# Kernel tuning notes

Measured on AMD Instinct MI355X. Metric: run time of the kernel, lower is better.

Reference implementation:

```python
import jax, jax.numpy as jnp
import numpy as np

B, T, C = 4, 2048, 1024
H = 16
D = C // H  # head_dim = 64
SCALE = D ** -0.5


def setup_inputs() -> dict:
    key = jax.random.key(0)
    k1, k2, k3 = jax.random.split(key, 3)
    x = jax.random.normal(k1, (B, T, C), dtype=jnp.float32)
    w_qkv = jax.random.normal(k2, (C, 3 * C), dtype=jnp.float32) * (C ** -0.5)
    w_proj = jax.random.normal(k3, (C, C), dtype=jnp.float32) * (C ** -0.5)
    return {"x": x, "w_qkv": w_qkv, "w_proj": w_proj}


def reference(x, w_qkv, w_proj):
    Bx, Tx, Cx = x.shape
    qkv = x @ w_qkv                        # [B, T, 3C]
    q, k, v = jnp.split(qkv, 3, axis=-1)   # each [B, T, C]
    # [B, T, H, D] -> [B, H, T, D]
    q = q.reshape(Bx, Tx, H, D).transpose(0, 2, 1, 3)
    k = k.reshape(Bx, Tx, H, D).transpose(0, 2, 1, 3)
    v = v.reshape(Bx, Tx, H, D).transpose(0, 2, 1, 3)
    att = jnp.einsum('bhqd,bhkd->bhqk', q, k) * SCALE  # [B, H, T, T]
    causal = jnp.tril(jnp.ones((Tx, Tx), dtype=bool))
    att = jnp.where(causal[None, None], att, -jnp.inf)
    att = jax.nn.softmax(att, axis=-1)
    # dropout p=0.0 (eval-mode reference): identity
    y = jnp.einsum('bhqk,bhkd->bhqd', att, v)          # [B, H, T, D]
    y = y.transpose(0, 2, 1, 3).reshape(Bx, Tx, Cx)    # [B, T, C]
    return y @ w_proj
```

## Files before the change

kernel.cpp:

```cpp
#include <hip/hip_runtime.h>
#include <hip/hip_bf16.h>

#define Bdim 4
#define Tdim 2048
#define Cdim 1024
#define Hdim 16
#define Ddim 64
#define SCALE_Q 0.125f

using f32x4  = __attribute__((ext_vector_type(4))) float;
using short8 = __attribute__((ext_vector_type(8))) short;

union U8 { uint4 v; unsigned short s[8]; };

__device__ __forceinline__ float bf2f(unsigned short u) {
  union { unsigned int i; float f; } x; x.i = ((unsigned int)u) << 16; return x.f;
}
__device__ __forceinline__ unsigned short f2bf(float f) {
  union { float f; unsigned int i; } x; x.f = f;
  unsigned int lsb = (x.i >> 16) & 1u;
  unsigned int r = x.i + 0x7fffu + lsb;
  return (unsigned short)(r >> 16);
}

__device__ __forceinline__ void glds16(const unsigned short* g, unsigned short* l) {
  __builtin_amdgcn_global_load_lds(
      (const __attribute__((address_space(1))) void*)g,
      (__attribute__((address_space(3))) void*)l,
      16, 0, 0);
}

__global__ void detect_kernel(const unsigned int* __restrict__ x, int* __restrict__ flag) {
  if (threadIdx.x == 0) {
    int cnt = 0;
    for (int i = 0; i < 64; i++) {
      unsigned int e = (x[i] >> 7) & 0xFFu;
      if (e >= 100u && e <= 140u) cnt++;
    }
    *flag = (cnt >= 40) ? 1 : 0;
  }
}

__global__ __launch_bounds__(256) void cvt_kernel(
    const void* __restrict__ src, unsigned short* __restrict__ dst,
    const int* __restrict__ flag, size_t n8)
{
  const size_t i = (size_t)blockIdx.x * 256 + threadIdx.x;
  if (i >= n8) return;
  if (*flag == 1) {
    *(uint4*)(dst + i * 8) = *(const uint4*)((const unsigned short*)src + i * 8);
  } else {
    const float* s = (const float*)src + i * 8;
    float4 a = *(const float4*)(s);
    float4 b = *(const float4*)(s + 4);
    U8 o;
    o.s[0]=f2bf(a.x); o.s[1]=f2bf(a.y); o.s[2]=f2bf(a.z); o.s[3]=f2bf(a.w);
    o.s[4]=f2bf(b.x); o.s[5]=f2bf(b.y); o.s[6]=f2bf(b.z); o.s[7]=f2bf(b.w);
    *(uint4*)(dst + i * 8) = o.v;
  }
}

__global__ __launch_bounds__(256) void cvtT_kernel(
    const void* __restrict__ W, unsigned short* __restrict__ WT,
    const int* __restrict__ flag, int K, int N)
{
  __shared__ __align__(16) unsigned short Ts[64][72];
  const int fmt = *flag;
  const int tid = threadIdx.x;
  const int n0 = blockIdx.x * 64, k0 = blockIdx.y * 64;
  const int r = tid >> 2, c0 = (tid & 3) * 16;

  if (fmt == 0) {
    const float* Wf = (const float*)W + (size_t)(k0 + r) * N + n0 + c0;
    #pragma unroll
    for (int j4 = 0; j4 < 4; j4++) {
      float4 v = *(const float4*)(Wf + j4 * 4);
      Ts[r][c0 + j4*4 + 0] = f2bf(v.x);
      Ts[r][c0 + j4*4 + 1] = f2bf(v.y);
      Ts[r][c0 + j4*4 + 2] = f2bf(v.z);
      Ts[r][c0 + j4*4 + 3] = f2bf(v.w);
    }
  } else {
    const unsigned short* Wh = (const unsigned short*)W + (size_t)(k0 + r) * N + n0 + c0;
    uint4 v0 = *(const uint4*)(Wh);
    uint4 v1 = *(const uint4*)(Wh + 8);
    *(uint4*)&Ts[r][c0] = v0;
    *(uint4*)&Ts[r][c0 + 8] = v1;
  }
  __syncthreads();

  U8 o0, o1;
  #pragma unroll
  for (int j = 0; j < 8; j++) { o0.s[j] = Ts[c0 + j][r]; o1.s[j] = Ts[c0 + 8 + j][r]; }
  unsigned short* dst = WT + (size_t)(n0 + r) * K + k0 + c0;
  *(uint4*)(dst)     = o0.v;
  *(uint4*)(dst + 8) = o1.v;
}

__global__ __launch_bounds__(256) void vtrans_kernel(
    const unsigned short* __restrict__ Vb, unsigned short* __restrict__ VbT)
{
  __shared__ __align__(16) unsigned short Ts[64][72];
  const int tid = threadIdx.x;
  const int head = blockIdx.x >> 5;
  const int tt   = blockIdx.x & 31;
  const int r = tid >> 2, c0 = (tid & 3) * 16;

  const unsigned short* src = Vb + (size_t)head * Tdim * Ddim + (size_t)(tt * 64 + r) * Ddim + c0;
  uint4 a = *(const uint4*)(src);
  uint4 b = *(const uint4*)(src + 8);
  *(uint4*)&Ts[r][c0]     = a;
  *(uint4*)&Ts[r][c0 + 8] = b;
  __syncthreads();

  U8 o0, o1;
  #pragma unroll
  for (int j = 0; j < 8; j++) { o0.s[j] = Ts[c0 + j][r]; o1.s[j] = Ts[c0 + 8 + j][r]; }
  unsigned short* dst = VbT + (size_t)head * Tdim * Ddim + (size_t)r * Tdim + tt * 64 + c0;
  *(uint4*)(dst)     = o0.v;
  *(uint4*)(dst + 8) = o1.v;
}

__global__ __launch_bounds__(256) void gemm128a_kernel(
    const unsigned short* __restrict__ A16,
    const unsigned short* __restrict__ BT16,
    void* __restrict__ Cout,
    unsigned short* __restrict__ Qb,
    unsigned short* __restrict__ Kb,
    unsigned short* __restrict__ Vb,
    const int* __restrict__ flag,
    int M, int N, int K, int mode)
{
  __shared__ __align__(16) unsigned short As[128 * 32];
  __shared__ __align__(16) unsigned short Bs[128 * 32];

  const int fmt = *flag;
  const int tid  = threadIdx.x;
  const int wave = tid >> 6;
  const int lane = tid & 63;
  const int col  = lane & 15;
  const int quad = lane >> 4;
  const int m0 = blockIdx.x * 128;
  const int n0 = blockIdx.y * 128;
  const int wm = (wave >> 1) * 64;
  const int wn = (wave & 1) * 64;

  const int lr = lane >> 2;
  const int lc = (lane & 3) * 8;

  f32x4 acc[4][4];
  #pragma unroll
  for (int i = 0; i < 4; i++)
    #pragma unroll
    for (int j = 0; j < 4; j++) acc[i][j] = (f32x4){0.f, 0.f, 0.f, 0.f};

  for (int k0 = 0; k0 < K; k0 += 32) {
    #pragma unroll
    for (int j = 0; j < 2; j++) {
      const int row = wave * 32 + j * 16;
      glds16(A16  + (size_t)(m0 + row + lr) * K + k0 + lc, &As[row * 32]);
      glds16(BT16 + (size_t)(n0 + row + lr) * K + k0 + lc, &Bs[row * 32]);
    }
    __syncthreads();

    short8 afr[4], bfr[4];
    #pragma unroll
    for (int mi = 0; mi < 4; mi++)
      afr[mi] = *(const short8*)&As[(wm + mi * 16 + col) * 32 + quad * 8];
    #pragma unroll
    for (int ni = 0; ni < 4; ni++)
      bfr[ni] = *(const short8*)&Bs[(wn + ni * 16 + col) * 32 + quad * 8];
    #pragma unroll
    for (int mi = 0; mi < 4; mi++)
      #pragma unroll
      for (int ni = 0; ni < 4; ni++)
        acc[mi][ni] = __builtin_amdgcn_mfma_f32_16x16x32_bf16(afr[mi], bfr[ni], acc[mi][ni], 0, 0, 0);
    __syncthreads();
  }

  #pragma unroll
  for (int mi = 0; mi < 4; mi++) {
    #pragma unroll
    for (int ni = 0; ni < 4; ni++) {
      #pragma unroll
      for (int i = 0; i < 4; i++) {
        const int m = m0 + wm + mi * 16 + quad * 4 + i;
        const int n = n0 + wn + ni * 16 + col;
        const float v = acc[mi][ni][i];
        if (mode == 0) {
          if (fmt == 0) ((float*)Cout)[(size_t)m * N + n] = v;
          else ((unsigned short*)Cout)[(size_t)m * N + n] = f2bf(v);
        } else {
          const int which = n >> 10;
          const int rem = n & 1023;
          const int h = rem >> 6;
          const int d = rem & 63;
          const int b = m >> 11;
          const int t = m & 2047;
          const size_t idx = ((size_t)(b * Hdim + h) * Tdim + t) * Ddim + d;
          if      (which == 0) Qb[idx] = f2bf(v * SCALE_Q);
          else if (which == 1) Kb[idx] = f2bf(v);
          else                 Vb[idx] = f2bf(v);
        }
      }
    }
  }
}

#define XBM 128
#define XBN 128
#define XBK 32
#define XLDK 40

__global__ __launch_bounds__(256) void gemm128_kernel(
    const unsigned short* __restrict__ A16,
    const void* __restrict__ Bsrc,
    void* __restrict__ Cout,
    unsigned short* __restrict__ Qb,
    unsigned short* __restrict__ Kb,
    unsigned short* __restrict__ Vb,
    const int* __restrict__ flag,
    int M, int N, int K, int mode, int bFmt)
{
  __shared__ __align__(16) unsigned short As[XBM * XLDK];
  __shared__ __align__(16) unsigned short Bs[XBN * XLDK];

  const int fmt = *flag;
  const int tid  = threadIdx.x;
  const int wave = tid >> 6;
  const int lane = tid & 63;
  const int col  = lane & 15;
  const int quad = lane >> 4;
  const int m0 = blockIdx.x * XBM;
  const int n0 = blockIdx.y * XBN;
  const int wm = (wave >> 1) * 64;
  const int wn = (wave & 1) * 64;

  const int ar = tid >> 1;
  const int ah = (tid & 1) * 16;

  f32x4 acc[4][4];
  #pragma unroll
  for (int i = 0; i < 4; i++)
    #pragma unroll
    for (int j = 0; j < 4; j++) acc[i][j] = (f32x4){0.f, 0.f, 0.f, 0.f};

  for (int k0 = 0; k0 < K; k0 += XBK) {
    {
      const unsigned short* Ap = A16 + (size_t)(m0 + ar) * K + k0 + ah;
      uint4 a0 = *(const uint4*)(Ap);
      uint4 a1 = *(const uint4*)(Ap + 8);
      *(uint4*)&As[ar * XLDK + ah]     = a0;
      *(uint4*)&As[ar * XLDK + ah + 8] = a1;
    }
    if (bFmt == 1) {
      const unsigned short* Bp = (const unsigned short*)Bsrc + (size_t)(n0 + ar) * K + k0 + ah;
      uint4 b0 = *(const uint4*)(Bp);
      uint4 b1 = *(const uint4*)(Bp + 8);
      *(uint4*)&Bs[ar * XLDK + ah]     = b0;
      *(uint4*)&Bs[ar * XLDK + ah + 8] = b1;
    } else {
      const int bn = tid & 127;
      const int bg = (tid >> 7) * 16;
      U8 p0, p1;
      if (fmt == 0) {
        const float* Bf = (const float*)Bsrc;
        #pragma unroll
        for (int j = 0; j < 8; j++) {
          p0.s[j] = f2bf(Bf[(size_t)(k0 + bg + j) * N + n0 + bn]);
          p1.s[j] = f2bf(Bf[(size_t)(k0 + bg + 8 + j) * N + n0 + bn]);
        }
      } else {
        const unsigned short* Bh = (const unsigned short*)Bsrc;
        #pragma unroll
        for (int j = 0; j < 8; j++) {
          p0.s[j] = Bh[(size_t)(k0 + bg + j) * N + n0 + bn];
          p1.s[j] = Bh[(size_t)(k0 + bg + 8 + j) * N + n0 + bn];
        }
      }
      *(uint4*)&Bs[bn * XLDK + bg]     = p0.v;
      *(uint4*)&Bs[bn * XLDK + bg + 8] = p1.v;
    }
    __syncthreads();

    short8 afr[4], bfr[4];
    #pragma unroll
    for (int mi = 0; mi < 4; mi++)
      afr[mi] = *(const short8*)&As[(wm + mi * 16 + col) * XLDK + quad * 8];
    #pragma unroll
    for (int ni = 0; ni < 4; ni++)
      bfr[ni] = *(const short8*)&Bs[(wn + ni * 16 + col) * XLDK + quad * 8];
    #pragma unroll
    for (int mi = 0; mi < 4; mi++)
      #pragma unroll
      for (int ni = 0; ni < 4; ni++)
        acc[mi][ni] = __builtin_amdgcn_mfma_f32_16x16x32_bf16(afr[mi], bfr[ni], acc[mi][ni], 0, 0, 0);
    __syncthreads();
  }

  #pragma unroll
  for (int mi = 0; mi < 4; mi++) {
    #pragma unroll
    for (int ni = 0; ni < 4; ni++) {
      #pragma unroll
      for (int i = 0; i < 4; i++) {
        const int m = m0 + wm + mi * 16 + quad * 4 + i;
        const int n = n0 + wn + ni * 16 + col;
        const float v = acc[mi][ni][i];
        if (mode == 0) {
          if (fmt == 0) ((float*)Cout)[(size_t)m * N + n] = v;
          else ((unsigned short*)Cout)[(size_t)m * N + n] = f2bf(v);
        } else {
          const int which = n >> 10;
          const int rem = n & 1023;
          const int h = rem >> 6;
          const int d = rem & 63;
          const int b = m >> 11;
          const int t = m & 2047;
          const size_t idx = ((size_t)(b * Hdim + h) * Tdim + t) * Ddim + d;
          if      (which == 0) Qb[idx] = f2bf(v * SCALE_Q);
          else if (which == 1) Kb[idx] = f2bf(v);
          else                 Vb[idx] = f2bf(v);
        }
      }
    }
  }
}

#define BM 64
#define BN 64
#define BK 32
#define LDK 40

__global__ __launch_bounds__(256) void gemm64_kernel(
    const void* __restrict__ A,
    const void* __restrict__ Bw,
    void* __restrict__ Cout,
    unsigned short* __restrict__ Qb,
    unsigned short* __restrict__ Kb,
    unsigned short* __restrict__ Vb,
    const int* __restrict__ flag,
    int M, int N, int K, int mode, int aFmt, int outFmt, int aOff, int mOff)
{
  __shared__ __align__(16) unsigned short As[BM * LDK];
  __shared__ __align__(16) unsigned short Bs[BN * LDK];

  const int fmt = *flag;
  const int af  = (aFmt  == 2) ? fmt : aFmt;
  const int of  = (outFmt == 2) ? fmt : outFmt;

  const int tid  = threadIdx.x;
  const int wave = tid >> 6;
  const int lane = tid & 63;
  const int m0 = blockIdx.x * BM;
  const int n0 = blockIdx.y * BN;

  const int ar = tid >> 2;
  const int ak = (tid & 3) * 8;
  const int bk = tid >> 3;
  const int bn = (tid & 7) * 8;

  const int lr = lane & 15;
  const int lq = lane >> 4;

  f32x4 acc[4] = {{0,0,0,0},{0,0,0,0},{0,0,0,0},{0,0,0,0}};

  for (int k0 = 0; k0 < K; k0 += BK) {
    U8 a8;
    if (af == 1) {
      a8.v = *(const uint4*)((const unsigned short*)A + (size_t)(aOff + m0 + ar) * K + (k0 + ak));
    } else {
      const float* Af = (const float*)A + (size_t)(aOff + m0 + ar) * K + (k0 + ak);
      float4 x0 = *(const float4*)(Af);
      float4 x1 = *(const float4*)(Af + 4);
      a8.s[0] = f2bf(x0.x); a8.s[1] = f2bf(x0.y); a8.s[2] = f2bf(x0.z); a8.s[3] = f2bf(x0.w);
      a8.s[4] = f2bf(x1.x); a8.s[5] = f2bf(x1.y); a8.s[6] = f2bf(x1.z); a8.s[7] = f2bf(x1.w);
    }
    *(uint4*)(&As[ar * LDK + ak]) = a8.v;

    U8 b8;
    if (fmt == 1) {
      b8.v = *(const uint4*)((const unsigned short*)Bw + (size_t)(k0 + bk) * N + (n0 + bn));
    } else {
      const float* Bf = (const float*)Bw + (size_t)(k0 + bk) * N + (n0 + bn);
      float4 x0 = *(const float4*)(Bf);
      float4 x1 = *(const float4*)(Bf + 4);
      b8.s[0] = f2bf(x0.x); b8.s[1] = f2bf(x0.y); b8.s[2] = f2bf(x0.z); b8.s[3] = f2bf(x0.w);
      b8.s[4] = f2bf(x1.x); b8.s[5] = f2bf(x1.y); b8.s[6] = f2bf(x1.z); b8.s[7] = f2bf(x1.w);
    }
    #pragma unroll
    for (int i = 0; i < 8; i++) Bs[(bn + i) * LDK + bk] = b8.s[i];
    __syncthreads();

    short8 afrag = *(const short8*)(&As[(wave * 16 + lr) * LDK + lq * 8]);
    #pragma unroll
    for (int c = 0; c < 4; c++) {
      short8 bfrag = *(const short8*)(&Bs[(c * 16 + lr) * LDK + lq * 8]);
      acc[c] = __builtin_amdgcn_mfma_f32_16x16x32_bf16(afrag, bfrag, acc[c], 0, 0, 0);
    }
    __syncthreads();
  }

  #pragma unroll
  for (int c = 0; c < 4; c++) {
    #pragma unroll
    for (int i = 0; i < 4; i++) {
      const int m = m0 + wave * 16 + lq * 4 + i;
      const int n = n0 + c * 16 + lr;
      const float v = acc[c][i];
      if (mode == 0) {
        if (of == 0) ((float*)Cout)[(size_t)(mOff + m) * N + n] = v;
        else ((unsigned short*)Cout)[(size_t)(mOff + m) * N + n] = f2bf(v);
      } else {
        const int which = n >> 10;
        const int rem = n & 1023;
        const int h = rem >> 6;
        const int d = rem & 63;
        const int b = m >> 11;
        const int t = m & 2047;
        const size_t idx = ((size_t)(b * Hdim + h) * Tdim + t) * Ddim + d;
        if      (which == 0) Qb[idx] = f2bf(v * SCALE_Q);
        else if (which == 1) Kb[idx] = f2bf(v);
        else                 Vb[idx] = f2bf(v);
      }
    }
  }
}

__global__ __launch_bounds__(256) void attn128_kernel(
    const unsigned short* __restrict__ Qb,
    const unsigned short* __restrict__ Kb,
    const unsigned short* __restrict__ Vb,
    const unsigned short* __restrict__ VbT,
    unsigned short* __restrict__ Y)
{
  __shared__ __align__(16) unsigned short Ks[64 * 72];
  __shared__ __align__(16) unsigned short Vt[64 * 72];
  __shared__ __align__(16) unsigned short Pw[4][32 * 72];

  const int tid  = threadIdx.x;
  const int wave = tid >> 6;
  const int lane = tid & 63;
  const int col  = lane & 15;
  const int quad = lane >> 4;

  const int pair = blockIdx.x & 7;
  const int bh   = blockIdx.x >> 3;
  const size_t headOff = (size_t)bh * Tdim * Ddim;

  const int sr = tid >> 2;
  const int sc = (tid & 3) * 16;

  const int b = bh >> 4;
  const int h = bh & 15;

  #pragma unroll
  for (int half = 0; half < 2; half++) {
    const int qt = half ? (15 - pair) : pair;
    const int qb = qt * 128;
    const int nkt = (qb >> 6) + 2;
    const int rMin = qb + wave * 32;
    const int rMax = rMin + 31;

    short8 qf[2][2];
    #pragma unroll
    for (int mi = 0; mi < 2; mi++) {
      const unsigned short* Qr = Qb + headOff + (size_t)(rMin + mi * 16 + col) * Ddim;
      qf[mi][0] = *(const short8*)(Qr + quad * 8);
      qf[mi][1] = *(const short8*)(Qr + 32 + quad * 8);
    }

    f32x4 o_acc[2][4];
    float l_i[2][4];
    #pragma unroll
    for (int mi = 0; mi < 2; mi++)
      #pragma unroll
      for (int n = 0; n < 4; n++) {
        o_acc[mi][n] = (f32x4){0.f, 0.f, 0.f, 0.f};
        l_i[mi][n] = 0.f;
      }

    uint4 kr0, kr1, vr0, vr1;
    {
      const unsigned short* Kr = Kb + headOff + (size_t)sr * Ddim + sc;
      kr0 = *(const uint4*)(Kr);
      kr1 = *(const uint4*)(Kr + 8);
      if (VbT) {
        const unsigned short* Vr = VbT + headOff + (size_t)sr * Tdim + sc;
        vr0 = *(const uint4*)(Vr);
        vr1 = *(const uint4*)(Vr + 8);
      } else {
        const unsigned short* Vr = Vb + headOff + (size_t)sr * Ddim + sc;
        vr0 = *(const uint4*)(Vr);
        vr1 = *(const uint4*)(Vr + 8);
      }
    }

    for (int kt = 0; kt < nkt; kt++) {
      __syncthreads();
      *(uint4*)&Ks[sr * 72 + sc]     = kr0;
      *(uint4*)&Ks[sr * 72 + sc + 8] = kr1;
      if (VbT) {
        *(uint4*)&Vt[sr * 72 + sc]     = vr0;
        *(uint4*)&Vt[sr * 72 + sc + 8] = vr1;
      } else {
        U8 v0, v1; v0.v = vr0; v1.v = vr1;
        #pragma unroll
        for (int j = 0; j < 8; j++) {
          Vt[(sc + j) * 72 + sr]     = v0.s[j];
          Vt[(sc + 8 + j) * 72 + sr] = v1.s[j];
        }
      }
      __syncthreads();

      if (kt + 1 < nkt) {
        const int kb = (kt + 1) * 64;
        const unsigned short* Kr = Kb + headOff + (size_t)(kb + sr) * Ddim + sc;
        kr0 = *(const uint4*)(Kr);
        kr1 = *(const uint4*)(Kr + 8);
        if (VbT) {
          const unsigned short* Vr = VbT + headOff + (size_t)sr * Tdim + kb + sc;
          vr0 = *(const uint4*)(Vr);
          vr1 = *(const uint4*)(Vr + 8);
        } else {
          const unsigned short* Vr = Vb + headOff + (size_t)(kb + sr) * Ddim + sc;
          vr0 = *(const uint4*)(Vr);
          vr1 = *(const uint4*)(Vr + 8);
        }
      }

      const int ktb = kt * 64;
      if (ktb <= rMax) {
        f32x4 s_acc[2][4];
        #pragma unroll
        for (int c = 0; c < 4; c++) {
          const unsigned short* Kl = &Ks[(c * 16 + col) * 72];
          short8 kf0 = *(const short8*)(Kl + quad * 8);
          short8 kf1 = *(const short8*)(Kl + 32 + quad * 8);
          #pragma unroll
          for (int mi = 0; mi < 2; mi++) {
            f32x4 z = {0.f, 0.f, 0.f, 0.f};
            z = __builtin_amdgcn_mfma_f32_16x16x32_bf16(qf[mi][0], kf0, z, 0, 0, 0);
            s_acc[mi][c] = __builtin_amdgcn_mfma_f32_16x16x32_bf16(qf[mi][1], kf1, z, 0, 0, 0);
          }
        }

        if (ktb + 63 > rMin) {
          #pragma unroll
          for (int mi = 0; mi < 2; mi++)
            #pragma unroll
            for (int c = 0; c < 4; c++)
              #pragma unroll
              for (int i = 0; i < 4; i++)
                if (ktb + c * 16 + col > rMin + mi * 16 + quad * 4 + i)
                  s_acc[mi][c][i] = -1e30f;
        }

        #pragma unroll
        for (int mi = 0; mi < 2; mi++)
          #pragma unroll
          for (int c = 0; c < 4; c++)
            #pragma unroll
            for (int i = 0; i < 4; i++) {
              const float p = __expf(fminf(s_acc[mi][c][i], 60.f));
              l_i[mi][i] += p;
              Pw[wave][(mi * 16 + quad * 4 + i) * 72 + c * 16 + col] = f2bf(p);
            }

        short8 pf[2][2];
        #pragma unroll
        for (int mi = 0; mi < 2; mi++) {
          pf[mi][0] = *(const short8*)(&Pw[wave][(mi * 16 + col) * 72 + quad * 8]);
          pf[mi][1] = *(const short8*)(&Pw[wave][(mi * 16 + col) * 72 + 32 + quad * 8]);
        }
        #pragma unroll
        for (int n = 0; n < 4; n++) {
          const unsigned short* Vl = &Vt[(n * 16 + col) * 72];
          short8 vf0 = *(const short8*)(Vl + quad * 8);
          short8 vf1 = *(const short8*)(Vl + 32 + quad * 8);
          #pragma unroll
          for (int mi = 0; mi < 2; mi++) {
            o_acc[mi][n] = __builtin_amdgcn_mfma_f32_16x16x32_bf16(pf[mi][0], vf0, o_acc[mi][n], 0, 0, 0);
            o_acc[mi][n] = __builtin_amdgcn_mfma_f32_16x16x32_bf16(pf[mi][1], vf1, o_acc[mi][n], 0, 0, 0);
          }
        }
      }
    }
    __syncthreads();

    #pragma unroll
    for (int mi = 0; mi < 2; mi++)
      #pragma unroll
      for (int i = 0; i < 4; i++) {
        float s = l_i[mi][i];
        s += __shfl_xor(s, 1);
        s += __shfl_xor(s, 2);
        s += __shfl_xor(s, 4);
        s += __shfl_xor(s, 8);
        const float inv = 1.f / s;
        const int qrow = rMin + mi * 16 + quad * 4 + i;
        unsigned short* dst = Y + (size_t)(b * Tdim + qrow) * Cdim + h * Ddim;
        #pragma unroll
        for (int n = 0; n < 4; n++)
          dst[n * 16 + col] = f2bf(o_acc[mi][n][i] * inv);
      }
  }
}

extern "C" void kernel_launch(void* const* d_in, const int* in_sizes, int n_in,
                              void* d_out, int out_size, void* d_ws, size_t ws_size,
                              hipStream_t stream) {
  const void* x      = d_in[0];
  const void* w_qkv  = d_in[1];
  const void* w_proj = d_in[2];

  int* flag = (int*)d_ws;
  unsigned short* wsb = (unsigned short*)((char*)d_ws + 1024);

  const size_t HS = (size_t)Bdim * Hdim * Tdim * Ddim;
  const size_t FULL  = 1024 + 2 * (4 * HS + (size_t)3072 * 1024 + (size_t)1024 * 1024);
  const size_t FULL2 = FULL + 2 * HS;
  const size_t MONO  = 1024 + 2 * (4 * HS);

  dim3 blk(256);
  detect_kernel<<<1, 64, 0, stream>>>((const unsigned int*)x, flag);

  if (ws_size >= MONO) {
    unsigned short* Qb  = wsb;
    unsigned short* Kb  = Qb + HS;
    unsigned short* Vb  = Kb + HS;
    unsigned short* XY  = Vb + HS;
    unsigned short* WqT = XY + HS;
    unsigned short* WpT = WqT + (size_t)3072 * 1024;
    unsigned short* VbT = WpT + (size_t)1024 * 1024;
    const int M = Bdim * Tdim;

    cvt_kernel<<<dim3((unsigned)((M * (size_t)Cdim / 8 + 255) / 256)), blk, 0, stream>>>(
        x, XY, flag, M * (size_t)Cdim / 8);

    if (ws_size >= FULL) {
      cvtT_kernel<<<dim3(3072 / 64, Cdim / 64), blk, 0, stream>>>(w_qkv, WqT, flag, Cdim, 3072);
      cvtT_kernel<<<dim3(Cdim / 64, Cdim / 64), blk, 0, stream>>>(w_proj, WpT, flag, Cdim, Cdim);

      gemm128a_kernel<<<dim3(M / 128, 3072 / 128), blk, 0, stream>>>(
          XY, WqT, nullptr, Qb, Kb, Vb, flag, M, 3072, Cdim, 1);

      if (ws_size >= FULL2) {
        vtrans_kernel<<<dim3(Bdim * Hdim * (Tdim / 64)), blk, 0, stream>>>(Vb, VbT);
        attn128_kernel<<<dim3(Bdim * Hdim * 8), blk, 0, stream>>>(Qb, Kb, Vb, VbT, XY);
      } else {
        attn128_kernel<<<dim3(Bdim * Hdim * 8), blk, 0, stream>>>(Qb, Kb, Vb, nullptr, XY);
      }

      gemm128a_kernel<<<dim3(M / 128, Cdim / 128), blk, 0, stream>>>(
          XY, WpT, d_out, nullptr, nullptr, nullptr, flag, M, Cdim, Cdim, 0);
    } else {
      gemm128_kernel<<<dim3(M / XBM, 3072 / XBN), blk, 0, stream>>>(
          XY, w_qkv, nullptr, Qb, Kb, Vb, flag, M, 3072, Cdim, 1, 0);

      attn128_kernel<<<dim3(Bdim * Hdim * 8), blk, 0, stream>>>(Qb, Kb, Vb, nullptr, XY);

      gemm128_kernel<<<dim3(M / XBM, Cdim / XBN), blk, 0, stream>>>(
          XY, w_proj, d_out, nullptr, nullptr, nullptr, flag, M, Cdim, Cdim, 0, 0);
    }
  } else {
    const size_t HSb = (size_t)Hdim * Tdim * Ddim;
    unsigned short* Qb = wsb;
    unsigned short* Kb = Qb + HSb;
    unsigned short* Vb = Kb + HSb;
    unsigned short* Y2 = Vb + HSb;

    for (int b = 0; b < Bdim; b++) {
      gemm64_kernel<<<dim3(Tdim / BM, 3072 / BN), blk, 0, stream>>>(
          x, w_qkv, nullptr, Qb, Kb, Vb, flag,
          Tdim, 3072, Cdim, 1, 2, 2, b * Tdim, 0);

      attn128_kernel<<<dim3(Hdim * 8), blk, 0, stream>>>(Qb, Kb, Vb, nullptr, Y2);

      gemm64_kernel<<<dim3(Tdim / BM, Cdim / BN), blk, 0, stream>>>(
          Y2, w_proj, d_out, nullptr, nullptr, nullptr, flag,
          Tdim, Cdim, Cdim, 0, 1, 2, 0, b * Tdim);
    }
  }
}
```

Baseline: 292.6 us.

## Fuse format detection and conversions into one prep kernel; widen GEMM K-step

Merges the detect, activation-convert and two weight-transpose kernels into a single prep kernel, removing three launches. The main GEMM now loads 64-wide K slices per barrier pair, split across two LDS halves, which halves the number of synchronizations. The QKV scatter epilogue hoists the head/destination computation out of the inner loop. The MONO fallback path was restructured to use the per-batch gemm64 path, and the unused gemm128 kernel is kept.

```diff
diff --git a/kernel.cpp b/kernel.cpp
--- a/kernel.cpp
+++ b/kernel.cpp
@@ -30,44 +30,62 @@
       16, 0, 0);
 }
 
+__device__ __forceinline__ int detect_fmt(const unsigned int* xw) {
+  int cnt = 0;
+  for (int i = 0; i < 64; i++) {
+    unsigned int e = (xw[i] >> 7) & 0xFFu;
+    if (e >= 100u && e <= 140u) cnt++;
+  }
+  return (cnt >= 40) ? 1 : 0;
+}
+
 __global__ void detect_kernel(const unsigned int* __restrict__ x, int* __restrict__ flag) {
-  if (threadIdx.x == 0) {
-    int cnt = 0;
-    for (int i = 0; i < 64; i++) {
-      unsigned int e = (x[i] >> 7) & 0xFFu;
-      if (e >= 100u && e <= 140u) cnt++;
-    }
-    *flag = (cnt >= 40) ? 1 : 0;
-  }
-}
-
-__global__ __launch_bounds__(256) void cvt_kernel(
-    const void* __restrict__ src, unsigned short* __restrict__ dst,
-    const int* __restrict__ flag, size_t n8)
-{
-  const size_t i = (size_t)blockIdx.x * 256 + threadIdx.x;
-  if (i >= n8) return;
-  if (*flag == 1) {
-    *(uint4*)(dst + i * 8) = *(const uint4*)((const unsigned short*)src + i * 8);
-  } else {
-    const float* s = (const float*)src + i * 8;
-    float4 a = *(const float4*)(s);
-    float4 b = *(const float4*)(s + 4);
-    U8 o;
-    o.s[0]=f2bf(a.x); o.s[1]=f2bf(a.y); o.s[2]=f2bf(a.z); o.s[3]=f2bf(a.w);
-    o.s[4]=f2bf(b.x); o.s[5]=f2bf(b.y); o.s[6]=f2bf(b.z); o.s[7]=f2bf(b.w);
-    *(uint4*)(dst + i * 8) = o.v;
-  }
-}
-
-__global__ __launch_bounds__(256) void cvtT_kernel(
-    const void* __restrict__ W, unsigned short* __restrict__ WT,
-    const int* __restrict__ flag, int K, int N)
+  if (threadIdx.x == 0) *flag = detect_fmt(x);
+}
+
+__global__ __launch_bounds__(256) void prep_kernel(
+    const void* __restrict__ x, const void* __restrict__ wq, const void* __restrict__ wp,
+    unsigned short* __restrict__ X16, unsigned short* __restrict__ WqT,
+    unsigned short* __restrict__ WpT, int* __restrict__ flag)
 {
   __shared__ __align__(16) unsigned short Ts[64][72];
-  const int fmt = *flag;
+  __shared__ int sfmt;
+  if (threadIdx.x == 0) {
+    const int f = detect_fmt((const unsigned int*)x);
+    sfmt = f;
+    if (blockIdx.x == 0) *flag = f;
+  }
+  __syncthreads();
+  const int fmt = sfmt;
+  const unsigned bid = blockIdx.x;
   const int tid = threadIdx.x;
-  const int n0 = blockIdx.x * 64, k0 = blockIdx.y * 64;
+
+  if (bid < 4096u) {
+    const size_t i = (size_t)bid * 256 + tid;
+    if (fmt == 1) {
+      *(uint4*)(X16 + i * 8) = *(const uint4*)((const unsigned short*)x + i * 8);
+    } else {
+      const float* s = (const float*)x + i * 8;
+      float4 a = *(const float4*)(s);
+      float4 b = *(const float4*)(s + 4);
+      U8 o;
+      o.s[0]=f2bf(a.x); o.s[1]=f2bf(a.y); o.s[2]=f2bf(a.z); o.s[3]=f2bf(a.w);
+      o.s[4]=f2bf(b.x); o.s[5]=f2bf(b.y); o.s[6]=f2bf(b.z); o.s[7]=f2bf(b.w);
+      *(uint4*)(X16 + i * 8) = o.v;
+    }
+    return;
+  }
+
+  const void* W; unsigned short* WT; int N, K, n0, k0;
+  if (bid < 4864u) {
+    const int t = bid - 4096;
+    W = wq; WT = WqT; N = 3072; K = 1024;
+    n0 = (t % 48) * 64; k0 = (t / 48) * 64;
+  } else {
+    const int t = bid - 4864;
+    W = wp; WT = WpT; N = 1024; K = 1024;
+    n0 = (t & 15) * 64; k0 = (t >> 4) * 64;
+  }
   const int r = tid >> 2, c0 = (tid & 3) * 16;
 
   if (fmt == 0) {
@@ -121,7 +139,7 @@
   *(uint4*)(dst + 8) = o1.v;
 }
 
-__global__ __launch_bounds__(256) void gemm128a_kernel(
+__global__ __launch_bounds__(256) void gemm128b_kernel(
     const unsigned short* __restrict__ A16,
     const unsigned short* __restrict__ BT16,
     void* __restrict__ Cout,
@@ -131,8 +149,8 @@
     const int* __restrict__ flag,
     int M, int N, int K, int mode)
 {
-  __shared__ __align__(16) unsigned short As[128 * 32];
-  __shared__ __align__(16) unsigned short Bs[128 * 32];
+  __shared__ __align__(16) unsigned short As[2][128 * 32];
+  __shared__ __align__(16) unsigned short Bs[2][128 * 32];
 
   const int fmt = *flag;
   const int tid  = threadIdx.x;
@@ -154,22 +172,165 @@
     #pragma unroll
     for (int j = 0; j < 4; j++) acc[i][j] = (f32x4){0.f, 0.f, 0.f, 0.f};
 
-  for (int k0 = 0; k0 < K; k0 += 32) {
-    #pragma unroll
-    for (int j = 0; j < 2; j++) {
-      const int row = wave * 32 + j * 16;
-      glds16(A16  + (size_t)(m0 + row + lr) * K + k0 + lc, &As[row * 32]);
-      glds16(BT16 + (size_t)(n0 + row + lr) * K + k0 + lc, &Bs[row * 32]);
-    }
+  const unsigned short* Ap0 = A16  + (size_t)(m0 + wave * 32 + lr) * K + lc;
+  const unsigned short* Ap1 = A16  + (size_t)(m0 + wave * 32 + 16 + lr) * K + lc;
+  const unsigned short* Bp0 = BT16 + (size_t)(n0 + wave * 32 + lr) * K + lc;
+  const unsigned short* Bp1 = BT16 + (size_t)(n0 + wave * 32 + 16 + lr) * K + lc;
+  unsigned short* a0 = &As[0][wave * 32 * 32];
+  unsigned short* a0b = &As[0][(wave * 32 + 16) * 32];
+  unsigned short* a1 = &As[1][wave * 32 * 32];
+  unsigned short* a1b = &As[1][(wave * 32 + 16) * 32];
+  unsigned short* b0 = &Bs[0][wave * 32 * 32];
+  unsigned short* b0b = &Bs[0][(wave * 32 + 16) * 32];
+  unsigned short* b1 = &Bs[1][wave * 32 * 32];
+  unsigned short* b1b = &Bs[1][(wave * 32 + 16) * 32];
+
+  for (int k0 = 0; k0 < K; k0 += 64) {
+    glds16(Ap0,      a0);  glds16(Ap0 + 32, a1);
+    glds16(Ap1,      a0b); glds16(Ap1 + 32, a1b);
+    glds16(Bp0,      b0);  glds16(Bp0 + 32, b1);
+    glds16(Bp1,      b0b); glds16(Bp1 + 32, b1b);
+    Ap0 += 64; Ap1 += 64; Bp0 += 64; Bp1 += 64;
     __syncthreads();
 
+    #pragma unroll
+    for (int half = 0; half < 2; half++) {
+      short8 afr[4], bfr[4];
+      #pragma unroll
+      for (int mi = 0; mi < 4; mi++)
+        afr[mi] = *(const short8*)&As[half][(wm + mi * 16 + col) * 32 + quad * 8];
+      #pragma unroll
+      for (int ni = 0; ni < 4; ni++)
+        bfr[ni] = *(const short8*)&Bs[half][(wn + ni * 16 + col) * 32 + quad * 8];
+      #pragma unroll
+      for (int mi = 0; mi < 4; mi++)
+        #pragma unroll
+        for (int ni = 0; ni < 4; ni++)
+          acc[mi][ni] = __builtin_amdgcn_mfma_f32_16x16x32_bf16(afr[mi], bfr[ni], acc[mi][ni], 0, 0, 0);
+    }
+    __syncthreads();
+  }
+
+  if (mode == 1) {
+    const int bb = m0 >> 11;
+    const int tBase = (m0 & 2047) + wm;
+    #pragma unroll
+    for (int ni = 0; ni < 4; ni++) {
+      const int n = n0 + wn + ni * 16 + col;
+      const int which = n >> 10;
+      const int rem = n & 1023;
+      const int h = rem >> 6;
+      const int d = rem & 63;
+      unsigned short* dstBase = (which == 0) ? Qb : (which == 1 ? Kb : Vb);
+      const float scale = (which == 0) ? SCALE_Q : 1.f;
+      dstBase += (size_t)(bb * Hdim + h) * Tdim * Ddim + d;
+      #pragma unroll
+      for (int mi = 0; mi < 4; mi++)
+        #pragma unroll
+        for (int i = 0; i < 4; i++) {
+          const int t = tBase + mi * 16 + quad * 4 + i;
+          dstBase[(size_t)t * Ddim] = f2bf(acc[mi][ni][i] * scale);
+        }
+    }
+  } else {
+    #pragma unroll
+    for (int mi = 0; mi < 4; mi++)
+      #pragma unroll
+      for (int ni = 0; ni < 4; ni++)
+        #pragma unroll
+        for (int i = 0; i < 4; i++) {
+          const int m = m0 + wm + mi * 16 + quad * 4 + i;
+          const int n = n0 + wn + ni * 16 + col;
+          const float v = acc[mi][ni][i];
+          if (fmt == 0) ((float*)Cout)[(size_t)m * N + n] = v;
+          else ((unsigned short*)Cout)[(size_t)m * N + n] = f2bf(v);
+        }
+  }
+}
+
+#define XBM 128
+#define XBN 128
+#define XBK 32
+#define XLDK 40
+
+__global__ __launch_bounds__(256) void gemm128_kernel(
+    const unsigned short* __restrict__ A16,
+    const void* __restrict__ Bsrc,
+    void* __restrict__ Cout,
+    unsigned short* __restrict__ Qb,
+    unsigned short* __restrict__ Kb,
+    unsigned short* __restrict__ Vb,
+    const int* __restrict__ flag,
+    int M, int N, int K, int mode, int bFmt)
+{
+  __shared__ __align__(16) unsigned short As[XBM * XLDK];
+  __shared__ __align__(16) unsigned short Bs[XBN * XLDK];
+
+  const int fmt = *flag;
+  const int tid  = threadIdx.x;
+  const int wave = tid >> 6;
+  const int lane = tid & 63;
+  const int col  = lane & 15;
+  const int quad = lane >> 4;
+  const int m0 = blockIdx.x * XBM;
+  const int n0 = blockIdx.y * XBN;
+  const int wm = (wave >> 1) * 64;
+  const int wn = (wave & 1) * 64;
+
+  const int ar = tid >> 1;
+  const int ah = (tid & 1) * 16;
+
+  f32x4 acc[4][4];
+  #pragma unroll
+  for (int i = 0; i < 4; i++)
+    #pragma unroll
+    for (int j = 0; j < 4; j++) acc[i][j] = (f32x4){0.f, 0.f, 0.f, 0.f};
+
+  for (int k0 = 0; k0 < K; k0 += XBK) {
+    {
+      const unsigned short* Ap = A16 + (size_t)(m0 + ar) * K + k0 + ah;
+      uint4 a0 = *(const uint4*)(Ap);
+      uint4 a1 = *(const uint4*)(Ap + 8);
+      *(uint4*)&As[ar * XLDK + ah]     = a0;
+      *(uint4*)&As[ar * XLDK + ah + 8] = a1;
+    }
+    if (bFmt == 1) {
+      const unsigned short* Bp = (const unsigned short*)Bsrc + (size_t)(n0 + ar) * K + k0 + ah;
+      uint4 b0 = *(const uint4*)(Bp);
+      uint4 b1 = *(const uint4*)(Bp + 8);
+      *(uint4*)&Bs[ar * XLDK + ah]     = b0;
+      *(uint4*)&Bs[ar * XLDK + ah + 8] = b1;
+    } else {
+      const int bn = tid & 127;
+      const int bg = (tid >> 7) * 16;
+      U8 p0, p1;
+      if (fmt == 0) {
+        const float* Bf = (const float*)Bsrc;
+        #pragma unroll
+        for (int j = 0; j < 8; j++) {
+          p0.s[j] = f2bf(Bf[(size_t)(k0 + bg + j) * N + n0 + bn]);
+          p1.s[j] = f2bf(Bf[(size_t)(k0 + bg + 8 + j) * N + n0 + bn]);
+        }
+      } else {
+        const unsigned short* Bh = (const unsigned short*)Bsrc;
+        #pragma unroll
+        for (int j = 0; j < 8; j++) {
+          p0.s[j] = Bh[(size_t)(k0 + bg + j) * N + n0 + bn];
+          p1.s[j] = Bh[(size_t)(k0 + bg + 8 + j) * N + n0 + bn];
+        }
+      }
+      *(uint4*)&Bs[bn * XLDK + bg]     = p0.v;
+      *(uint4*)&Bs[bn * XLDK + bg + 8] = p1.v;
+    }
+    __syncthreads();
+
     short8 afr[4], bfr[4];
     #pragma unroll
     for (int mi = 0; mi < 4; mi++)
-      afr[mi] = *(const short8*)&As[(wm + mi * 16 + col) * 32 + quad * 8];
+      afr[mi] = *(const short8*)&As[(wm + mi * 16 + col) * XLDK + quad * 8];
     #pragma unroll
     for (int ni = 0; ni < 4; ni++)
-      bfr[ni] = *(const short8*)&Bs[(wn + ni * 16 + col) * 32 + quad * 8];
+      bfr[ni] = *(const short8*)&Bs[(wn + ni * 16 + col) * XLDK + quad * 8];
     #pragma unroll
     for (int mi = 0; mi < 4; mi++)
       #pragma unroll
@@ -207,126 +368,6 @@
   }
 }
 
-#define XBM 128
-#define XBN 128
-#define XBK 32
-#define XLDK 40
-
-__global__ __launch_bounds__(256) void gemm128_kernel(
-    const unsigned short* __restrict__ A16,
-    const void* __restrict__ Bsrc,
-    void* __restrict__ Cout,
-    unsigned short* __restrict__ Qb,
-    unsigned short* __restrict__ Kb,
-    unsigned short* __restrict__ Vb,
-    const int* __restrict__ flag,
-    int M, int N, int K, int mode, int bFmt)
-{
-  __shared__ __align__(16) unsigned short As[XBM * XLDK];
-  __shared__ __align__(16) unsigned short Bs[XBN * XLDK];
-
-  const int fmt = *flag;
-  const int tid  = threadIdx.x;
-  const int wave = tid >> 6;
-  const int lane = tid & 63;
-  const int col  = lane & 15;
-  const int quad = lane >> 4;
-  const int m0 = blockIdx.x * XBM;
-  const int n0 = blockIdx.y * XBN;
-  const int wm = (wave >> 1) * 64;
-  const int wn = (wave & 1) * 64;
-
-  const int ar = tid >> 1;
-  const int ah = (tid & 1) * 16;
-
-  f32x4 acc[4][4];
-  #pragma unroll
-  for (int i = 0; i < 4; i++)
-    #pragma unroll
-    for (int j = 0; j < 4; j++) acc[i][j] = (f32x4){0.f, 0.f, 0.f, 0.f};
-
-  for (int k0 = 0; k0 < K; k0 += XBK) {
-    {
-      const unsigned short* Ap = A16 + (size_t)(m0 + ar) * K + k0 + ah;
-      uint4 a0 = *(const uint4*)(Ap);
-      uint4 a1 = *(const uint4*)(Ap + 8);
-      *(uint4*)&As[ar * XLDK + ah]     = a0;
-      *(uint4*)&As[ar * XLDK + ah + 8] = a1;
-    }
-    if (bFmt == 1) {
-      const unsigned short* Bp = (const unsigned short*)Bsrc + (size_t)(n0 + ar) * K + k0 + ah;
-      uint4 b0 = *(const uint4*)(Bp);
-      uint4 b1 = *(const uint4*)(Bp + 8);
-      *(uint4*)&Bs[ar * XLDK + ah]     = b0;
-      *(uint4*)&Bs[ar * XLDK + ah + 8] = b1;
-    } else {
-      const int bn = tid & 127;
-      const int bg = (tid >> 7) * 16;
-      U8 p0, p1;
-      if (fmt == 0) {
-        const float* Bf = (const float*)Bsrc;
-        #pragma unroll
-        for (int j = 0; j < 8; j++) {
-          p0.s[j] = f2bf(Bf[(size_t)(k0 + bg + j) * N + n0 + bn]);
-          p1.s[j] = f2bf(Bf[(size_t)(k0 + bg + 8 + j) * N + n0 + bn]);
-        }
-      } else {
-        const unsigned short* Bh = (const unsigned short*)Bsrc;
-        #pragma unroll
-        for (int j = 0; j < 8; j++) {
-          p0.s[j] = Bh[(size_t)(k0 + bg + j) * N + n0 + bn];
-          p1.s[j] = Bh[(size_t)(k0 + bg + 8 + j) * N + n0 + bn];
-        }
-      }
-      *(uint4*)&Bs[bn * XLDK + bg]     = p0.v;
-      *(uint4*)&Bs[bn * XLDK + bg + 8] = p1.v;
-    }
-    __syncthreads();
-
-    short8 afr[4], bfr[4];
-    #pragma unroll
-    for (int mi = 0; mi < 4; mi++)
-      afr[mi] = *(const short8*)&As[(wm + mi * 16 + col) * XLDK + quad * 8];
-    #pragma unroll
-    for (int ni = 0; ni < 4; ni++)
-      bfr[ni] = *(const short8*)&Bs[(wn + ni * 16 + col) * XLDK + quad * 8];
-    #pragma unroll
-    for (int mi = 0; mi < 4; mi++)
-      #pragma unroll
-      for (int ni = 0; ni < 4; ni++)
-        acc[mi][ni] = __builtin_amdgcn_mfma_f32_16x16x32_bf16(afr[mi], bfr[ni], acc[mi][ni], 0, 0, 0);
-    __syncthreads();
-  }
-
-  #pragma unroll
-  for (int mi = 0; mi < 4; mi++) {
-    #pragma unroll
-    for (int ni = 0; ni < 4; ni++) {
-      #pragma unroll
-      for (int i = 0; i < 4; i++) {
-        const int m = m0 + wm + mi * 16 + quad * 4 + i;
-        const int n = n0 + wn + ni * 16 + col;
-        const float v = acc[mi][ni][i];
-        if (mode == 0) {
-          if (fmt == 0) ((float*)Cout)[(size_t)m * N + n] = v;
-          else ((unsigned short*)Cout)[(size_t)m * N + n] = f2bf(v);
-        } else {
-          const int which = n >> 10;
-          const int rem = n & 1023;
-          const int h = rem >> 6;
-          const int d = rem & 63;
-          const int b = m >> 11;
-          const int t = m & 2047;
-          const size_t idx = ((size_t)(b * Hdim + h) * Tdim + t) * Ddim + d;
-          if      (which == 0) Qb[idx] = f2bf(v * SCALE_Q);
-          else if (which == 1) Kb[idx] = f2bf(v);
-          else                 Vb[idx] = f2bf(v);
-        }
-      }
-    }
-  }
-}
-
 #define BM 64
 #define BN 64
 #define BK 32
@@ -623,9 +664,8 @@
   const size_t MONO  = 1024 + 2 * (4 * HS);
 
   dim3 blk(256);
-  detect_kernel<<<1, 64, 0, stream>>>((const unsigned int*)x, flag);
-
-  if (ws_size >= MONO) {
+
+  if (ws_size >= FULL) {
     unsigned short* Qb  = wsb;
     unsigned short* Kb  = Qb + HS;
     unsigned short* Vb  = Kb + HS;
@@ -635,35 +675,50 @@
     unsigned short* VbT = WpT + (size_t)1024 * 1024;
     const int M = Bdim * Tdim;
 
-    cvt_kernel<<<dim3((unsigned)((M * (size_t)Cdim / 8 + 255) / 256)), blk, 0, stream>>>(
-        x, XY, flag, M * (size_t)Cdim / 8);
-
-    if (ws_size >= FULL) {
-      cvtT_kernel<<<dim3(3072 / 64, Cdim / 64), blk, 0, stream>>>(w_qkv, WqT, flag, Cdim, 3072);
-      cvtT_kernel<<<dim3(Cdim / 64, Cdim / 64), blk, 0, stream>>>(w_proj, WpT, flag, Cdim, Cdim);
-
-      gemm128a_kernel<<<dim3(M / 128, 3072 / 128), blk, 0, stream>>>(
-          XY, WqT, nullptr, Qb, Kb, Vb, flag, M, 3072, Cdim, 1);
-
-      if (ws_size >= FULL2) {
-        vtrans_kernel<<<dim3(Bdim * Hdim * (Tdim / 64)), blk, 0, stream>>>(Vb, VbT);
-        attn128_kernel<<<dim3(Bdim * Hdim * 8), blk, 0, stream>>>(Qb, Kb, Vb, VbT, XY);
-      } else {
-        attn128_kernel<<<dim3(Bdim * Hdim * 8), blk, 0, stream>>>(Qb, Kb, Vb, nullptr, XY);
-      }
-
-      gemm128a_kernel<<<dim3(M / 128, Cdim / 128), blk, 0, stream>>>(
-          XY, WpT, d_out, nullptr, nullptr, nullptr, flag, M, Cdim, Cdim, 0);
+    prep_kernel<<<dim3(5120), blk, 0, stream>>>(x, w_qkv, w_proj, XY, WqT, WpT, flag);
+
+    gemm128b_kernel<<<dim3(M / 128, 3072 / 128), blk, 0, stream>>>(
+        XY, WqT, nullptr, Qb, Kb, Vb, flag, M, 3072, Cdim, 1);
+
+    if (ws_size >= FULL2) {
+      vtrans_kernel<<<dim3(Bdim * Hdim * (Tdim / 64)), blk, 0, stream>>>(Vb, VbT);
+      attn128_kernel<<<dim3(Bdim * Hdim * 8), blk, 0, stream>>>(Qb, Kb, Vb, VbT, XY);
     } else {
-      gemm128_kernel<<<dim3(M / XBM, 3072 / XBN), blk, 0, stream>>>(
-          XY, w_qkv, nullptr, Qb, Kb, Vb, flag, M, 3072, Cdim, 1, 0);
-
       attn128_kernel<<<dim3(Bdim * Hdim * 8), blk, 0, stream>>>(Qb, Kb, Vb, nullptr, XY);
-
-      gemm128_kernel<<<dim3(M / XBM, Cdim / XBN), blk, 0, stream>>>(
-          XY, w_proj, d_out, nullptr, nullptr, nullptr, flag, M, Cdim, Cdim, 0, 0);
+    }
+
+    gemm128b_kernel<<<dim3(M / 128, Cdim / 128), blk, 0, stream>>>(
+        XY, WpT, d_out, nullptr, nullptr, nullptr, flag, M, Cdim, Cdim, 0);
+  } else if (ws_size >= MONO) {
+    unsigned short* Qb  = wsb;
+    unsigned short* Kb  = Qb + HS;
+    unsigned short* Vb  = Kb + HS;
+    unsigned short* XY  = Vb + HS;
+    const int M = Bdim * Tdim;
+
+    detect_kernel<<<1, 64, 0, stream>>>((const unsigned int*)x, flag);
+
+    {
+      const size_t n8 = (size_t)M * Cdim / 8;
+      (void)n8;
+    }
+
+    const size_t HSb = (size_t)Hdim * Tdim * Ddim;
+    unsigned short* Qb2 = wsb;
+    unsigned short* Kb2 = Qb2 + HSb;
+    unsigned short* Vb2 = Kb2 + HSb;
+    unsigned short* Y2  = Vb2 + HSb;
+    for (int b = 0; b < Bdim; b++) {
+      gemm64_kernel<<<dim3(Tdim / BM, 3072 / BN), blk, 0, stream>>>(
+          x, w_qkv, nullptr, Qb2, Kb2, Vb2, flag,
+          Tdim, 3072, Cdim, 1, 2, 2, b * Tdim, 0);
+      attn128_kernel<<<dim3(Hdim * 8), blk, 0, stream>>>(Qb2, Kb2, Vb2, nullptr, Y2);
+      gemm64_kernel<<<dim3(Tdim / BM, Cdim / BN), blk, 0, stream>>>(
+          Y2, w_proj, d_out, nullptr, nullptr, nullptr, flag,
+          Tdim, Cdim, Cdim, 0, 1, 2, 0, b * Tdim);
     }
   } else {
+    detect_kernel<<<1, 64, 0, stream>>>((const unsigned int*)x, flag);
     const size_t HSb = (size_t)Hdim * Tdim * Ddim;
     unsigned short* Qb = wsb;
     unsigned short* Kb = Qb + HSb;
```

After: 273.8 us. -6.4%, faster.
